# Optimization experiments

Hardware: AMD Instinct MI355X
Metric: run time of the kernel (lower is better)

The kernel has to match this reference:

```python
import jax, jax.numpy as jnp
import numpy as np

TAU = 1.0
K = 10
N_NODES = 1048576
N_GRAPHS = 4096


def setup_inputs() -> dict:
    key = jax.random.key(0)
    k1, k2, k3 = jax.random.split(key, 3)
    # per-node scalar logits
    x = jax.random.normal(k1, (N_NODES, 1), dtype=jnp.float32)
    # uniforms for gumbel noise, kept away from {0,1} for log stability
    uniforms = jax.random.uniform(k2, (N_NODES, 3 * K), dtype=jnp.float32,
                                  minval=1e-6, maxval=1.0 - 1e-6)
    # PyG-style ptr: B+1 cumulative offsets, ptr[0]=0, ptr[-1]=N
    cuts = jnp.sort(jax.random.randint(k3, (N_GRAPHS - 1,), 1, N_NODES))
    ptr = jnp.concatenate([jnp.zeros((1,), cuts.dtype), cuts,
                           jnp.full((1,), N_NODES, cuts.dtype)])
    return {"x": x, "uniforms": uniforms, "ptr": ptr}


def reference(x, uniforms, ptr):
    # x: [N, 1] node logits; uniforms: [N, 3k]; ptr: [B+1] segment offsets
    N = x.shape[0]
    B = ptr.shape[0] - 1
    # node i belongs to graph g where ptr[g] <= i < ptr[g+1]
    seg = jnp.searchsorted(ptr, jnp.arange(N), side="right") - 1  # [N]
    gumbel = -jnp.log(-jnp.log(uniforms))                           # [N, 3k]
    noisy = (gumbel + x) / TAU                                      # [N, 3k]
    # segmented softmax over nodes (dim=0 within each graph), per column
    m = jax.ops.segment_max(noisy, seg, num_segments=B)             # [B, 3k]
    e = jnp.exp(noisy - m[seg])                                     # [N, 3k]
    denom = jax.ops.segment_sum(e, seg, num_segments=B)             # [B, 3k]
    probs = e / denom[seg]                                          # [N, 3k]
    # max over the 3k gumbel samples per node
    samples = jnp.max(probs, axis=1)                                # [N]
    return samples[:, None]                                         # [N, 1]
```

## Files before the change

kernel.cpp:

```cpp
#include <hip/hip_runtime.h>

#define NK3 30
#define NKP 15

__device__ __forceinline__ float hw_log2(float a) { return __builtin_amdgcn_logf(a); }
__device__ __forceinline__ float hw_exp2(float a) { return __builtin_amdgcn_exp2f(a); }
__device__ __forceinline__ float hw_rcp(float a)  { return __builtin_amdgcn_rcpf(a); }

template <int CTRL>
__device__ __forceinline__ float dpp_add(float v) {
    int s = __builtin_amdgcn_update_dpp(0, __float_as_int(v), CTRL, 0xF, 0xF, true);
    return v + __int_as_float(s);
}
__device__ __forceinline__ float group16_sum(float v) {
    v = dpp_add<0xB1>(v);
    v = dpp_add<0x4E>(v);
    v = dpp_add<0x141>(v);
    v = dpp_add<0x140>(v);
    return v;
}
__device__ __forceinline__ float wave64_sum_hi(float v) {
    v = group16_sum(v);
    v = dpp_add<0x142>(v);
    v = dpp_add<0x143>(v);
    return v;
}


__global__ __launch_bounds__(256) void k1_window_sums(
    const float* __restrict__ x, const float* __restrict__ uniforms,
    float* __restrict__ wpart, int N)
{
    const int w    = (blockIdx.x << 2) + (threadIdx.x >> 6);
    const int lane = threadIdx.x & 63;
    const int base = w << 6;
    if (base >= N) return;

    const int n  = base + lane;
    const int nv = (n < N) ? n : (N - 1);

    const float2* row = reinterpret_cast<const float2*>(uniforms + (size_t)nv * NK3);
    float2 u[NKP];
#pragma unroll
    for (int k = 0; k < NKP; ++k) u[k] = row[k];
    float E = hw_exp2(x[nv] * 1.44269504f);
    E = (n < N) ? E : 0.0f;

    float r[NK3];
#pragma unroll
    for (int k = 0; k < NKP; ++k) {
        r[2 * k]     = E * hw_rcp(-hw_log2(u[k].x));
        r[2 * k + 1] = E * hw_rcp(-hw_log2(u[k].y));
    }

#pragma unroll
    for (int j = 0; j < NK3; ++j) r[j] = wave64_sum_hi(r[j]);

    if (lane == 63) {
        float* dst = wpart + (size_t)w * NK3;
#pragma unroll
        for (int j = 0; j < NK3; ++j) dst[j] = r[j];
    }
}

__global__ __launch_bounds__(256) void k2_segment_den(
    const float* __restrict__ x, const float* __restrict__ uniforms,
    const int* __restrict__ ptr, const float* __restrict__ wpart,
    float* __restrict__ den, int B)
{
    const int s = (blockIdx.x << 2) + (threadIdx.x >> 6);
    if (s >= B) return;
    const int lane = threadIdx.x & 63;
    const int h  = lane >> 5;
    const int j  = lane & 31;
    const bool jact = (j < NK3);
    const int jc = jact ? j : 0;

    const int start = ptr[s];
    const int end   = ptr[s + 1];

    const int wlo = (start + 63) >> 6;
    const int whi = end >> 6;
    const int head_end = min(wlo << 6, end);
    const int tail_beg = max(whi << 6, head_end);

    float acc = 0.0f;

    for (int w = wlo + h; w < whi; w += 2)
        acc += wpart[(size_t)w * NK3 + jc];

    for (int n = start + h; n < head_end; n += 2) {
        const float E = hw_exp2(x[n] * 1.44269504f);
        const float uv = uniforms[(size_t)n * NK3 + jc];
        acc = fmaf(E, hw_rcp(-hw_log2(uv)), acc);
    }
    for (int n = tail_beg + h; n < end; n += 2) {
        const float E = hw_exp2(x[n] * 1.44269504f);
        const float uv = uniforms[(size_t)n * NK3 + jc];
        acc = fmaf(E, hw_rcp(-hw_log2(uv)), acc);
    }

    acc += __shfl_xor(acc, 32, 64);

    if (h == 0 && jact) den[(size_t)s * NK3 + j] = acc;
}

__global__ __launch_bounds__(256) void k3_output(
    const float* __restrict__ x, const float* __restrict__ uniforms,
    const int* __restrict__ ptr, const float* __restrict__ den,
    float* __restrict__ out, int N, int B)
{
    const int wid  = (blockIdx.x << 2) + (threadIdx.x >> 6);
    const int lane = threadIdx.x & 63;
    const int base = wid << 8;
    if (base >= N) return;

    const int n0 = base + lane;
    int lo = 0, hi = B;
    while (hi - lo > 1) { int mid = (lo + hi) >> 1; if (ptr[mid] <= n0) lo = mid; else hi = mid; }
    int seg = lo;

    for (int c = 0; c < 4; ++c) {
        const int n = base + (c << 6) + lane;
        if (n >= N) return;
        while (n >= ptr[seg + 1]) ++seg;

        float l[NK3];
#pragma unroll
        for (int j = 0; j < NK3; ++j) l[j] = hw_rcp(den[(size_t)seg * NK3 + j]);

        const float2* row = reinterpret_cast<const float2*>(uniforms + (size_t)n * NK3);
        float mx = 0.0f;
#pragma unroll
        for (int k = 0; k < NKP; ++k) {
            const float2 u = row[k];
            const float r0 = hw_rcp(-hw_log2(u.x));
            const float r1 = hw_rcp(-hw_log2(u.y));
            mx = fmaxf(mx, fmaxf(r0 * l[2 * k], r1 * l[2 * k + 1]));
        }
        out[n] = hw_exp2(x[n] * 1.44269504f) * mx;
    }
}

__global__ __launch_bounds__(256) void gnn_fallback(
    const float* __restrict__ x, const float* __restrict__ uniforms,
    const int* __restrict__ ptr, float* __restrict__ out)
{
    const int wave = threadIdx.x >> 6;
    const int lane = threadIdx.x & 63;
    const int g = (blockIdx.x << 2) + wave;
    const int start = ptr[g];
    const int end   = ptr[g + 1];
    if (end <= start) return;

    float acc[NK3];
#pragma unroll
    for (int j = 0; j < NK3; ++j) acc[j] = 0.0f;
    const int iters = (end - start + 63) >> 6;

    for (int it = 0; it < iters; ++it) {
        const int n = start + (it << 6) + lane;
        if (n < end) {
            const float E = hw_exp2(x[n] * 1.44269504f);
            const float2* row = reinterpret_cast<const float2*>(uniforms + (size_t)n * NK3);
#pragma unroll
            for (int k = 0; k < NKP; ++k) {
                float2 u = row[k];
                acc[2 * k]     = fmaf(E, hw_rcp(-hw_log2(u.x)), acc[2 * k]);
                acc[2 * k + 1] = fmaf(E, hw_rcp(-hw_log2(u.y)), acc[2 * k + 1]);
            }
        }
    }
#pragma unroll
    for (int j = 0; j < NK3; ++j) {
        float v = acc[j];
#pragma unroll
        for (int off = 1; off < 64; off <<= 1) v += __shfl_xor(v, off, 64);
        acc[j] = hw_rcp(v);
    }
    for (int it = 0; it < iters; ++it) {
        const int n = start + (it << 6) + lane;
        if (n < end) {
            const float2* row = reinterpret_cast<const float2*>(uniforms + (size_t)n * NK3);
            float mx = 0.0f;
#pragma unroll
            for (int k = 0; k < NKP; ++k) {
                float2 u = row[k];
                const float r0 = hw_rcp(-hw_log2(u.x));
                const float r1 = hw_rcp(-hw_log2(u.y));
                mx = fmaxf(mx, fmaxf(r0 * acc[2 * k], r1 * acc[2 * k + 1]));
            }
            out[n] = hw_exp2(x[n] * 1.44269504f) * mx;
        }
    }
}

extern "C" void kernel_launch(void* const* d_in, const int* in_sizes, int n_in,
                              void* d_out, int out_size, void* d_ws, size_t ws_size,
                              hipStream_t stream) {
    const float* x        = (const float*)d_in[0];
    const float* uniforms = (const float*)d_in[1];
    const int*   ptr      = (const int*)d_in[2];
    float* out = (float*)d_out;

    const int N = in_sizes[0];
    const int B = in_sizes[2] - 1;
    const int NW = (N + 63) / 64;
    const size_t ws_needed = ((size_t)NW + (size_t)B) * NK3 * sizeof(float);

    if (ws_size >= ws_needed && d_ws != nullptr) {
        float* wpart = (float*)d_ws;
        float* den   = wpart + (size_t)NW * NK3;

        const int b1 = (NW + 3) / 4;
        k1_window_sums<<<b1, 256, 0, stream>>>(x, uniforms, wpart, N);

        const int b2 = (B + 3) / 4;
        k2_segment_den<<<b2, 256, 0, stream>>>(x, uniforms, ptr, wpart, den, B);

        const int b3 = (N + 1023) / 1024;
        k3_output<<<b3, 256, 0, stream>>>(x, uniforms, ptr, den, out, N, B);
    } else {
        const int blocks = (B + 3) / 4;
        gnn_fallback<<<blocks, 256, 0, stream>>>(x, uniforms, ptr, out);
    }
}
```

Before: 76.39 us.

## Use 16-node partial sums and multi-chunk waves; cache per-segment reciprocals

The first kernel now reduces each column only within groups of 16 lanes and writes partial sums at 16-node granularity, which drops the two cross-row DPP steps. Each wave now handles four 64-node chunks, so the grid is four times smaller. Finer windows mean the segment kernel computes fewer boundary nodes directly from uniforms, since head and tail shrink below 16 nodes. In exchange it must sum four times as many partials, and the first kernel writes four times more workspace. The output kernel reloads and inverts the 30 denominators only when the segment changes between chunks.

```diff
diff --git a/kernel.cpp b/kernel.cpp
--- a/kernel.cpp
+++ b/kernel.cpp
@@ -19,53 +19,51 @@
     v = dpp_add<0x140>(v);
     return v;
 }
-__device__ __forceinline__ float wave64_sum_hi(float v) {
-    v = group16_sum(v);
-    v = dpp_add<0x142>(v);
-    v = dpp_add<0x143>(v);
-    return v;
-}
 
 
 __global__ __launch_bounds__(256) void k1_window_sums(
     const float* __restrict__ x, const float* __restrict__ uniforms,
-    float* __restrict__ wpart, int N)
-{
-    const int w    = (blockIdx.x << 2) + (threadIdx.x >> 6);
-    const int lane = threadIdx.x & 63;
-    const int base = w << 6;
-    if (base >= N) return;
-
-    const int n  = base + lane;
-    const int nv = (n < N) ? n : (N - 1);
-
-    const float2* row = reinterpret_cast<const float2*>(uniforms + (size_t)nv * NK3);
-    float2 u[NKP];
-#pragma unroll
-    for (int k = 0; k < NKP; ++k) u[k] = row[k];
-    float E = hw_exp2(x[nv] * 1.44269504f);
-    E = (n < N) ? E : 0.0f;
-
-    float r[NK3];
-#pragma unroll
-    for (int k = 0; k < NKP; ++k) {
-        r[2 * k]     = E * hw_rcp(-hw_log2(u[k].x));
-        r[2 * k + 1] = E * hw_rcp(-hw_log2(u[k].y));
-    }
-
-#pragma unroll
-    for (int j = 0; j < NK3; ++j) r[j] = wave64_sum_hi(r[j]);
-
-    if (lane == 63) {
-        float* dst = wpart + (size_t)w * NK3;
-#pragma unroll
-        for (int j = 0; j < NK3; ++j) dst[j] = r[j];
+    float* __restrict__ wp16, int N)
+{
+    const int wid  = (blockIdx.x << 2) + (threadIdx.x >> 6);
+    const int lane = threadIdx.x & 63;
+    const int base0 = wid << 8;
+    if (base0 >= N) return;
+
+    for (int c = 0; c < 4; ++c) {
+        const int base = base0 + (c << 6);
+        if (base >= N) return;
+        const int n  = base + lane;
+        const int nv = (n < N) ? n : (N - 1);
+
+        const float2* row = reinterpret_cast<const float2*>(uniforms + (size_t)nv * NK3);
+        float2 u[NKP];
+#pragma unroll
+        for (int k = 0; k < NKP; ++k) u[k] = row[k];
+        float E = hw_exp2(x[nv] * 1.44269504f);
+        E = (n < N) ? E : 0.0f;
+
+        float r[NK3];
+#pragma unroll
+        for (int k = 0; k < NKP; ++k) {
+            r[2 * k]     = E * hw_rcp(-hw_log2(u[k].x));
+            r[2 * k + 1] = E * hw_rcp(-hw_log2(u[k].y));
+        }
+
+#pragma unroll
+        for (int j = 0; j < NK3; ++j) r[j] = group16_sum(r[j]);
+
+        if ((lane & 15) == 0) {
+            float* dst = wp16 + ((size_t)(base >> 4) + (lane >> 4)) * NK3;
+#pragma unroll
+            for (int j = 0; j < NK3; ++j) dst[j] = r[j];
+        }
     }
 }
 
 __global__ __launch_bounds__(256) void k2_segment_den(
     const float* __restrict__ x, const float* __restrict__ uniforms,
-    const int* __restrict__ ptr, const float* __restrict__ wpart,
+    const int* __restrict__ ptr, const float* __restrict__ wp16,
     float* __restrict__ den, int B)
 {
     const int s = (blockIdx.x << 2) + (threadIdx.x >> 6);
@@ -79,15 +77,15 @@
     const int start = ptr[s];
     const int end   = ptr[s + 1];
 
-    const int wlo = (start + 63) >> 6;
-    const int whi = end >> 6;
-    const int head_end = min(wlo << 6, end);
-    const int tail_beg = max(whi << 6, head_end);
+    const int wlo = (start + 15) >> 4;
+    const int whi = end >> 4;
+    const int head_end = min(wlo << 4, end);
+    const int tail_beg = max(whi << 4, head_end);
 
     float acc = 0.0f;
 
     for (int w = wlo + h; w < whi; w += 2)
-        acc += wpart[(size_t)w * NK3 + jc];
+        acc += wp16[(size_t)w * NK3 + jc];
 
     for (int n = start + h; n < head_end; n += 2) {
         const float E = hw_exp2(x[n] * 1.44269504f);
@@ -120,14 +118,19 @@
     while (hi - lo > 1) { int mid = (lo + hi) >> 1; if (ptr[mid] <= n0) lo = mid; else hi = mid; }
     int seg = lo;
 
+    int cur = -1;
+    float l[NK3];
+
     for (int c = 0; c < 4; ++c) {
         const int n = base + (c << 6) + lane;
         if (n >= N) return;
         while (n >= ptr[seg + 1]) ++seg;
 
-        float l[NK3];
-#pragma unroll
-        for (int j = 0; j < NK3; ++j) l[j] = hw_rcp(den[(size_t)seg * NK3 + j]);
+        if (seg != cur) {
+            cur = seg;
+#pragma unroll
+            for (int j = 0; j < NK3; ++j) l[j] = hw_rcp(den[(size_t)seg * NK3 + j]);
+        }
 
         const float2* row = reinterpret_cast<const float2*>(uniforms + (size_t)n * NK3);
         float mx = 0.0f;
@@ -205,18 +208,18 @@
 
     const int N = in_sizes[0];
     const int B = in_sizes[2] - 1;
-    const int NW = (N + 63) / 64;
-    const size_t ws_needed = ((size_t)NW + (size_t)B) * NK3 * sizeof(float);
+    const int NW16 = (N + 15) / 16;
+    const size_t ws_needed = ((size_t)NW16 + (size_t)B) * NK3 * sizeof(float);
 
     if (ws_size >= ws_needed && d_ws != nullptr) {
-        float* wpart = (float*)d_ws;
-        float* den   = wpart + (size_t)NW * NK3;
-
-        const int b1 = (NW + 3) / 4;
-        k1_window_sums<<<b1, 256, 0, stream>>>(x, uniforms, wpart, N);
+        float* wp16 = (float*)d_ws;
+        float* den  = wp16 + (size_t)NW16 * NK3;
+
+        const int b1 = (N + 1023) / 1024;
+        k1_window_sums<<<b1, 256, 0, stream>>>(x, uniforms, wp16, N);
 
         const int b2 = (B + 3) / 4;
-        k2_segment_den<<<b2, 256, 0, stream>>>(x, uniforms, ptr, wpart, den, B);
+        k2_segment_den<<<b2, 256, 0, stream>>>(x, uniforms, ptr, wp16, den, B);
 
         const int b3 = (N + 1023) / 1024;
         k3_output<<<b3, 256, 0, stream>>>(x, uniforms, ptr, den, out, N, B);
```

Result: faster. 70.23 us (-8.1%).
